# Kernel tuning notes

Measured on AMD Instinct MI355X. Metric: run time of the kernel, lower is better.

## Reference

```python
import jax, jax.numpy as jnp
import numpy as np

B, N, D = 1, 512, 128


def setup_inputs() -> dict:
    key = jax.random.key(0)
    ks = jax.random.split(key, 8)
    h = jax.random.normal(ks[0], (B, N, D), dtype=jnp.float32)
    rel_emb = jax.random.normal(ks[1], (B, N, N, D), dtype=jnp.float32)
    edge_mask = jax.random.bernoulli(ks[2], 0.5, (B, N, N))
    s2d = 1.0 / np.sqrt(2 * D)
    s1d = 1.0 / np.sqrt(D)
    return {
        "h": h,
        "rel_emb": rel_emb,
        "edge_mask": edge_mask,
        "msg_w1": jax.random.normal(ks[3], (2 * D, D), dtype=jnp.float32) * s2d,
        "msg_b1": jnp.zeros((D,), jnp.float32),
        "msg_w2": jax.random.normal(ks[4], (D, D), dtype=jnp.float32) * s1d,
        "msg_b2": jnp.zeros((D,), jnp.float32),
        "upd_w1": jax.random.normal(ks[5], (2 * D, D), dtype=jnp.float32) * s2d,
        "upd_b1": jnp.zeros((D,), jnp.float32),
        "upd_w2": jax.random.normal(ks[6], (D, D), dtype=jnp.float32) * s1d,
        "upd_b2": jnp.zeros((D,), jnp.float32),
        "ln_g": jnp.ones((D,), jnp.float32),
        "ln_b": jnp.zeros((D,), jnp.float32),
    }


def _layernorm(x, g, b, eps=1e-5):
    mu = x.mean(-1, keepdims=True)
    var = x.var(-1, keepdims=True)
    return (x - mu) * jax.lax.rsqrt(var + eps) * g + b


def reference(h, rel_emb, edge_mask, msg_w1, msg_b1, msg_w2, msg_b2,
              upd_w1, upd_b1, upd_w2, upd_b2, ln_g, ln_b):
    _, n, d = h.shape
    # msg_in = cat([h_j, e_ji]); h_j[b,i,j] = h[b,j], e_ji[b,i,j] = rel_emb[b,j,i]
    # Split first linear so the h-dependent part is computed once per sender j.
    w1_h, w1_e = msg_w1[:d], msg_w1[d:]
    hj_part = h @ w1_h                                   # [B,N,D], indexed by sender j
    e_ji = jnp.swapaxes(rel_emb, 1, 2)                   # [B,N(i),N(j),D]
    pre = hj_part[:, None, :, :] + jnp.einsum('bijd,de->bije', e_ji, w1_e) + msg_b1
    msgs = jax.nn.silu(pre) @ msg_w2 + msg_b2            # [B,N,N,D]
    mask = jnp.swapaxes(edge_mask, 1, 2).astype(h.dtype)  # [B,N(i),N(j)]
    agg = jnp.einsum('bijd,bij->bid', msgs, mask)        # masked sum over senders j
    upd_in = jnp.concatenate([h, agg], axis=-1)          # [B,N,2D]
    delta = jax.nn.silu(upd_in @ upd_w1 + upd_b1) @ upd_w2 + upd_b2
    return _layernorm(h + delta, ln_g, ln_b)
```

## Files before the change

kernel.cpp:

```cpp
#include <hip/hip_runtime.h>
#include <hip/hip_bf16.h>

#define NN 512
#define DD 128

typedef __bf16 bf16x8 __attribute__((ext_vector_type(8)));
typedef float f32x4 __attribute__((ext_vector_type(4)));

static __device__ __forceinline__ f32x4 mfma16(bf16x8 a, bf16x8 b, f32x4 c) {
  return __builtin_amdgcn_mfma_f32_16x16x32_bf16(a, b, c, 0, 0, 0);
}

__global__ void k_pre(const float* __restrict__ h,
                      const float* __restrict__ msg_w1,
                      const float* __restrict__ msg_b1,
                      const int* __restrict__ emask,
                      __bf16* __restrict__ w1t, float* __restrict__ hjp,
                      float* __restrict__ cnt) {
  __shared__ float hr[128];
  __shared__ int csum;
  int j = blockIdx.x, t = threadIdx.x;
  if (t == 0) csum = 0;
  hr[t] = h[j * 128 + t];
  __syncthreads();
  float acc = msg_b1[t];
  #pragma unroll 16
  for (int k = 0; k < 128; k++) acc += hr[k] * msg_w1[k * 128 + t];
  hjp[j * 128 + t] = acc;
  if (t < 32) {
    int tt = j * 32 + t;
    int e = tt >> 7, k = tt & 127;
    w1t[e * 128 + k] = (__bf16)msg_w1[(128 + k) * 128 + e];
  }
  int s = 0;
  #pragma unroll
  for (int r = 0; r < 4; r++) s += emask[(t * 4 + r) * NN + j] ? 1 : 0;
  #pragma unroll
  for (int off = 32; off > 0; off >>= 1) s += __shfl_down(s, off, 64);
  if ((t & 63) == 0) atomicAdd(&csum, s);
  __syncthreads();
  if (t == 0) cnt[j] = (float)csum;
}

#define CVT(bf, xa, xb) { \
  bf[0] = (__bf16)xa[0]; bf[1] = (__bf16)xa[1]; \
  bf[2] = (__bf16)xa[2]; bf[3] = (__bf16)xa[3]; \
  bf[4] = (__bf16)xb[0]; bf[5] = (__bf16)xb[1]; \
  bf[6] = (__bf16)xb[2]; bf[7] = (__bf16)xb[3]; }

__global__ __launch_bounds__(256, 2) void k_main(
    const float* __restrict__ rel, const int* __restrict__ emask,
    const float* __restrict__ hjp, const __bf16* __restrict__ w1t_g,
    float* __restrict__ partial) {
  __shared__ __align__(16) __bf16 tile[2 * 16 * 136];
  const int tid = threadIdx.x;
  const int wave = tid >> 6;
  const int lane = tid & 63;
  const int l15 = lane & 15;
  const int q = lane >> 4;

  const int it = blockIdx.x >> 5;
  const int jc = blockIdx.x & 31;
  const int irow = it * 16;
  const int jbase = jc * 16;

  bf16x8 aw00, aw01, aw02, aw03, aw10, aw11, aw12, aw13;
  {
    const __bf16* b0 = w1t_g + (wave * 32 + l15) * 128 + q * 8;
    aw00 = *(const bf16x8*)(b0);
    aw01 = *(const bf16x8*)(b0 + 32);
    aw02 = *(const bf16x8*)(b0 + 64);
    aw03 = *(const bf16x8*)(b0 + 96);
    const __bf16* b1 = b0 + 16 * 128;
    aw10 = *(const bf16x8*)(b1);
    aw11 = *(const bf16x8*)(b1 + 32);
    aw12 = *(const bf16x8*)(b1 + 64);
    aw13 = *(const bf16x8*)(b1 + 96);
  }

  f32x4 t0 = {0.f, 0.f, 0.f, 0.f}, t1 = t0;

  const int srow = tid >> 4;
  const int schunk = tid & 15;
  const float* sb = rel + ((size_t)jbase * NN + irow + srow) * DD + schunk * 8;
  __bf16* sd = tile + srow * 136 + schunk * 8;
  const size_t emrow = (size_t)irow + srow;

  f32x4 xa = {0.f, 0.f, 0.f, 0.f}, xb = xa;
  {
    float msw = emask[(size_t)jbase * NN + emrow] ? 1.f : 0.f;
    if (msw != 0.f) { xa = *(const f32x4*)sb; xb = *(const f32x4*)(sb + 4); }
    bf16x8 pub;
    CVT(pub, xa, xb)
    *(bf16x8*)sd = pub;
    msw = emask[(size_t)(jbase + 1) * NN + emrow] ? 1.f : 0.f;
    if (msw != 0.f) {
      const float* s = sb + (size_t)NN * DD;
      xa = *(const f32x4*)s;
      xb = *(const f32x4*)(s + 4);
    }
  }

  #pragma unroll 1
  for (int jj = 0; jj < 16; ++jj) {
    __syncthreads();

    if (jj < 15) {
      bf16x8 pub;
      CVT(pub, xa, xb)
      *(bf16x8*)(sd + (((jj + 1) & 1) ? 2176 : 0)) = pub;
    }
    if (jj < 14) {
      float msw = emask[(size_t)(jbase + jj + 2) * NN + emrow] ? 1.f : 0.f;
      if (msw != 0.f) {
        const float* s = sb + (size_t)(jj + 2) * NN * DD;
        xa = *(const f32x4*)s;
        xb = *(const f32x4*)(s + 4);
      }
    }

    const int j = jbase + jj;
    const float ms = emask[(size_t)j * NN + irow + l15] ? 1.f : 0.f;
    const __bf16* tp = tile + ((jj & 1) ? 2176 : 0) + l15 * 136 + q * 8;
    bf16x8 bf0 = *(const bf16x8*)(tp);
    bf16x8 bf1 = *(const bf16x8*)(tp + 32);
    bf16x8 bf2 = *(const bf16x8*)(tp + 64);
    bf16x8 bf3 = *(const bf16x8*)(tp + 96);
    f32x4 p0 = {0.f, 0.f, 0.f, 0.f}, p1 = p0;
    p0 = mfma16(aw00, bf0, p0); p1 = mfma16(aw10, bf0, p1);
    p0 = mfma16(aw01, bf1, p0); p1 = mfma16(aw11, bf1, p1);
    p0 = mfma16(aw02, bf2, p0); p1 = mfma16(aw12, bf2, p1);
    p0 = mfma16(aw03, bf3, p0); p1 = mfma16(aw13, bf3, p1);
    const float* hj = hjp + (size_t)j * DD + wave * 32 + q * 4;
    f32x4 hv0 = *(const f32x4*)(hj);
    f32x4 hv1 = *(const f32x4*)(hj + 16);
    #pragma unroll
    for (int r = 0; r < 4; r++) {
      float v0 = p0[r] + hv0[r];
      float v1 = p1[r] + hv1[r];
      t0[r] += ms * v0 * __builtin_amdgcn_rcpf(1.f + __expf(-v0));
      t1[r] += ms * v1 * __builtin_amdgcn_rcpf(1.f + __expf(-v1));
    }
  }

  float* pp = partial + ((size_t)jc * NN + irow + l15) * DD + wave * 32 + q * 4;
  *(f32x4*)pp = t0;
  *(f32x4*)(pp + 16) = t1;
}

__global__ void k_update(const float* __restrict__ h, const float* __restrict__ partial,
                         const float* __restrict__ w2, const float* __restrict__ b2,
                         const float* __restrict__ cnt,
                         const float* __restrict__ uw1, const float* __restrict__ ub1,
                         const float* __restrict__ uw2, const float* __restrict__ ub2,
                         const float* __restrict__ g, const float* __restrict__ bb,
                         float* __restrict__ out) {
  __shared__ float Trow[128];
  __shared__ float uin[256];
  __shared__ float zl[128];
  __shared__ float ss[4];
  int i = blockIdx.x, t = threadIdx.x;
  float hv = h[i * 128 + t];
  float ts = 0.f;
  #pragma unroll
  for (int c = 0; c < 32; c++) ts += partial[((size_t)c * NN + i) * DD + t];
  Trow[t] = ts;
  __syncthreads();
  float a = cnt[i] * b2[t];
  #pragma unroll 16
  for (int e = 0; e < 128; e++) a += Trow[e] * w2[e * 128 + t];
  uin[t] = hv;
  uin[128 + t] = a;
  __syncthreads();
  float z = ub1[t];
  #pragma unroll 16
  for (int k = 0; k < 256; k++) z += uin[k] * uw1[k * 128 + t];
  z = z / (1.f + __expf(-z));
  zl[t] = z;
  __syncthreads();
  float dl = ub2[t];
  #pragma unroll 16
  for (int k = 0; k < 128; k++) dl += zl[k] * uw2[k * 128 + t];
  float x = hv + dl;
  float s1 = x, s2 = x * x;
  #pragma unroll
  for (int off = 32; off > 0; off >>= 1) {
    s1 += __shfl_down(s1, off, 64);
    s2 += __shfl_down(s2, off, 64);
  }
  if ((t & 63) == 0) { ss[(t >> 6) * 2] = s1; ss[(t >> 6) * 2 + 1] = s2; }
  __syncthreads();
  s1 = ss[0] + ss[2];
  s2 = ss[1] + ss[3];
  float mu = s1 * (1.f / 128.f);
  float var = s2 * (1.f / 128.f) - mu * mu;
  out[i * 128 + t] = (x - mu) * rsqrtf(var + 1e-5f) * g[t] + bb[t];
}

extern "C" void kernel_launch(void* const* d_in, const int* in_sizes, int n_in,
                              void* d_out, int out_size, void* d_ws, size_t ws_size,
                              hipStream_t stream) {
  const float* h      = (const float*)d_in[0];
  const float* rel    = (const float*)d_in[1];
  const int*   emask  = (const int*)d_in[2];
  const float* msg_w1 = (const float*)d_in[3];
  const float* msg_b1 = (const float*)d_in[4];
  const float* msg_w2 = (const float*)d_in[5];
  const float* msg_b2 = (const float*)d_in[6];
  const float* upd_w1 = (const float*)d_in[7];
  const float* upd_b1 = (const float*)d_in[8];
  const float* upd_w2 = (const float*)d_in[9];
  const float* upd_b2 = (const float*)d_in[10];
  const float* ln_g   = (const float*)d_in[11];
  const float* ln_b   = (const float*)d_in[12];
  float* out = (float*)d_out;

  char* ws = (char*)d_ws;
  float*  hjp     = (float*)ws;
  __bf16* w1t     = (__bf16*)(ws + 262144);
  float*  cnt     = (float*)(ws + 262144 + 32768);
  float*  partial = (float*)(ws + 262144 + 36864);

  k_pre<<<512, 128, 0, stream>>>(h, msg_w1, msg_b1, emask, w1t, hjp, cnt);
  k_main<<<1024, 256, 0, stream>>>(rel, emask, hjp, w1t, partial);
  k_update<<<512, 128, 0, stream>>>(h, partial, msg_w2, msg_b2, cnt,
                                    upd_w1, upd_b1, upd_w2, upd_b2,
                                    ln_g, ln_b, out);
}
```

Before: 49.84 us.

## Prefetch rel_emb two steps ahead and stage edge mask in LDS

The main message kernel now loads the block's 16x16 edge-mask tile into shared memory once, rather than re-reading the global mask for every sender step and every load decision. The sender loop is unrolled by two and keeps two register prefetch buffers, so the global load for the next tile is issued two iterations ahead of its use. The aim is to hide more global-memory latency on the masked rel_emb stream and to drop redundant mask reads. The cost is higher register pressure from the extra buffers, which could hurt occupancy, plus one additional barrier at kernel start.

```diff
diff --git a/kernel.cpp b/kernel.cpp
--- a/kernel.cpp
+++ b/kernel.cpp
@@ -53,6 +53,7 @@
     const float* __restrict__ hjp, const __bf16* __restrict__ w1t_g,
     float* __restrict__ partial) {
   __shared__ __align__(16) __bf16 tile[2 * 16 * 136];
+  __shared__ float mk[256];
   const int tid = threadIdx.x;
   const int wave = tid >> 6;
   const int lane = tid & 63;
@@ -63,6 +64,8 @@
   const int jc = blockIdx.x & 31;
   const int irow = it * 16;
   const int jbase = jc * 16;
+
+  mk[tid] = emask[(size_t)(jbase + (tid >> 4)) * NN + irow + (tid & 15)] ? 1.f : 0.f;
 
   bf16x8 aw00, aw01, aw02, aw03, aw10, aw11, aw12, aw13;
   {
@@ -84,64 +87,83 @@
   const int schunk = tid & 15;
   const float* sb = rel + ((size_t)jbase * NN + irow + srow) * DD + schunk * 8;
   __bf16* sd = tile + srow * 136 + schunk * 8;
-  const size_t emrow = (size_t)irow + srow;
-
-  f32x4 xa = {0.f, 0.f, 0.f, 0.f}, xb = xa;
+
+  __syncthreads();
+
+  f32x4 xa0 = {0.f, 0.f, 0.f, 0.f}, xb0 = xa0;
+  f32x4 xa1 = xa0, xb1 = xa0;
   {
-    float msw = emask[(size_t)jbase * NN + emrow] ? 1.f : 0.f;
-    if (msw != 0.f) { xa = *(const f32x4*)sb; xb = *(const f32x4*)(sb + 4); }
+    if (mk[srow] != 0.f) { xa0 = *(const f32x4*)sb; xb0 = *(const f32x4*)(sb + 4); }
     bf16x8 pub;
-    CVT(pub, xa, xb)
+    CVT(pub, xa0, xb0)
     *(bf16x8*)sd = pub;
-    msw = emask[(size_t)(jbase + 1) * NN + emrow] ? 1.f : 0.f;
-    if (msw != 0.f) {
+    xa0 = {0.f, 0.f, 0.f, 0.f}; xb0 = xa0;
+    if (mk[16 + srow] != 0.f) {
       const float* s = sb + (size_t)NN * DD;
-      xa = *(const f32x4*)s;
-      xb = *(const f32x4*)(s + 4);
-    }
-  }
+      xa0 = *(const f32x4*)s; xb0 = *(const f32x4*)(s + 4);
+    }
+    if (mk[32 + srow] != 0.f) {
+      const float* s = sb + 2 * (size_t)NN * DD;
+      xa1 = *(const f32x4*)s; xb1 = *(const f32x4*)(s + 4);
+    }
+  }
+
+  #define COMPUTE(JROW, BUFOFF) { \
+    const float ms = mk[(JROW) * 16 + l15]; \
+    const __bf16* tp = tile + (BUFOFF) + l15 * 136 + q * 8; \
+    bf16x8 bf0 = *(const bf16x8*)(tp); \
+    bf16x8 bf1 = *(const bf16x8*)(tp + 32); \
+    bf16x8 bf2 = *(const bf16x8*)(tp + 64); \
+    bf16x8 bf3 = *(const bf16x8*)(tp + 96); \
+    f32x4 p0 = {0.f, 0.f, 0.f, 0.f}, p1 = p0; \
+    p0 = mfma16(aw00, bf0, p0); p1 = mfma16(aw10, bf0, p1); \
+    p0 = mfma16(aw01, bf1, p0); p1 = mfma16(aw11, bf1, p1); \
+    p0 = mfma16(aw02, bf2, p0); p1 = mfma16(aw12, bf2, p1); \
+    p0 = mfma16(aw03, bf3, p0); p1 = mfma16(aw13, bf3, p1); \
+    const float* hj = hjp + (size_t)(jbase + (JROW)) * DD + wave * 32 + q * 4; \
+    f32x4 hv0 = *(const f32x4*)(hj); \
+    f32x4 hv1 = *(const f32x4*)(hj + 16); \
+    _Pragma("unroll") \
+    for (int r = 0; r < 4; r++) { \
+      float v0 = p0[r] + hv0[r]; \
+      float v1 = p1[r] + hv1[r]; \
+      t0[r] += ms * v0 * __builtin_amdgcn_rcpf(1.f + __expf(-v0)); \
+      t1[r] += ms * v1 * __builtin_amdgcn_rcpf(1.f + __expf(-v1)); \
+    } }
 
   #pragma unroll 1
-  for (int jj = 0; jj < 16; ++jj) {
+  for (int jj = 0; jj < 16; jj += 2) {
     __syncthreads();
-
-    if (jj < 15) {
+    {
       bf16x8 pub;
-      CVT(pub, xa, xb)
-      *(bf16x8*)(sd + (((jj + 1) & 1) ? 2176 : 0)) = pub;
-    }
-    if (jj < 14) {
-      float msw = emask[(size_t)(jbase + jj + 2) * NN + emrow] ? 1.f : 0.f;
-      if (msw != 0.f) {
-        const float* s = sb + (size_t)(jj + 2) * NN * DD;
-        xa = *(const f32x4*)s;
-        xb = *(const f32x4*)(s + 4);
+      CVT(pub, xa0, xb0)
+      *(bf16x8*)(sd + 2176) = pub;
+      if (jj + 3 < 16) {
+        if (mk[(jj + 3) * 16 + srow] != 0.f) {
+          const float* s = sb + (size_t)(jj + 3) * NN * DD;
+          xa0 = *(const f32x4*)s; xb0 = *(const f32x4*)(s + 4);
+        }
       }
     }
-
-    const int j = jbase + jj;
-    const float ms = emask[(size_t)j * NN + irow + l15] ? 1.f : 0.f;
-    const __bf16* tp = tile + ((jj & 1) ? 2176 : 0) + l15 * 136 + q * 8;
-    bf16x8 bf0 = *(const bf16x8*)(tp);
-    bf16x8 bf1 = *(const bf16x8*)(tp + 32);
-    bf16x8 bf2 = *(const bf16x8*)(tp + 64);
-    bf16x8 bf3 = *(const bf16x8*)(tp + 96);
-    f32x4 p0 = {0.f, 0.f, 0.f, 0.f}, p1 = p0;
-    p0 = mfma16(aw00, bf0, p0); p1 = mfma16(aw10, bf0, p1);
-    p0 = mfma16(aw01, bf1, p0); p1 = mfma16(aw11, bf1, p1);
-    p0 = mfma16(aw02, bf2, p0); p1 = mfma16(aw12, bf2, p1);
-    p0 = mfma16(aw03, bf3, p0); p1 = mfma16(aw13, bf3, p1);
-    const float* hj = hjp + (size_t)j * DD + wave * 32 + q * 4;
-    f32x4 hv0 = *(const f32x4*)(hj);
-    f32x4 hv1 = *(const f32x4*)(hj + 16);
-    #pragma unroll
-    for (int r = 0; r < 4; r++) {
-      float v0 = p0[r] + hv0[r];
-      float v1 = p1[r] + hv1[r];
-      t0[r] += ms * v0 * __builtin_amdgcn_rcpf(1.f + __expf(-v0));
-      t1[r] += ms * v1 * __builtin_amdgcn_rcpf(1.f + __expf(-v1));
-    }
-  }
+    COMPUTE(jj, 0)
+
+    __syncthreads();
+    {
+      if (jj + 2 < 16) {
+        bf16x8 pub;
+        CVT(pub, xa1, xb1)
+        *(bf16x8*)sd = pub;
+      }
+      if (jj + 4 < 16) {
+        if (mk[(jj + 4) * 16 + srow] != 0.f) {
+          const float* s = sb + (size_t)(jj + 4) * NN * DD;
+          xa1 = *(const f32x4*)s; xb1 = *(const f32x4*)(s + 4);
+        }
+      }
+    }
+    COMPUTE(jj + 1, 2176)
+  }
+  #undef COMPUTE
 
   float* pp = partial + ((size_t)jc * NN + irow + l15) * DD + wave * 32 + q * 4;
   *(f32x4*)pp = t0;
```

Result: faster. 46.31 us (-7.1%).
